# Performance work log

Measured on AMD Instinct MI355X. Metric: run time of the kernel, lower is better.

The kernel has to match this reference:

```python
import jax, jax.numpy as jnp
import numpy as np

B, S, D, H = 2, 2048, 512, 8
HD = D // H
EPS = 1e-5


def _ln(x, g, b):
    mu = jnp.mean(x, axis=-1, keepdims=True)
    var = jnp.mean((x - mu) ** 2, axis=-1, keepdims=True)
    return (x - mu) * jax.lax.rsqrt(var + EPS) * g + b


def setup_inputs() -> dict:
    key = jax.random.key(0)
    ks = jax.random.split(key, 16)
    x = jax.random.normal(ks[0], (B, S, D), dtype=jnp.float32)
    adj = jax.random.randint(ks[1], (B, S, S), 0, 2, dtype=jnp.int32)
    adj = adj.at[:, jnp.arange(S), jnp.arange(S)].set(1)  # self-loops, avoid all-masked rows
    edge_attr = jax.random.normal(ks[2], (B, S, S), dtype=jnp.float32)
    sc = 1.0 / np.sqrt(D)
    p = lambda k, shp: jax.random.normal(k, shp, dtype=jnp.float32) * sc
    return {
        "x": x, "adj_matrix": adj, "edge_attr_matrix": edge_attr,
        "ln1_g": jnp.ones((D,)), "ln1_b": jnp.zeros((D,)),
        "ln2_g": jnp.ones((D,)), "ln2_b": jnp.zeros((D,)),
        "wq": p(ks[3], (D, D)), "bq": jnp.zeros((D,)),
        "wk": p(ks[4], (D, D)), "bk": jnp.zeros((D,)),
        "wv": p(ks[5], (D, D)), "bv": jnp.zeros((D,)),
        "wo": p(ks[6], (D, D)), "bo": jnp.zeros((D,)),
        "w1": p(ks[7], (D, 4 * D)), "b1": jnp.zeros((4 * D,)),
        "w2": p(ks[8], (4 * D, D)), "b2": jnp.zeros((D,)),
    }


def reference(x, adj_matrix, edge_attr_matrix, ln1_g, ln1_b, ln2_g, ln2_b,
              wq, bq, wk, bk, wv, bv, wo, bo, w1, b1, w2, b2):
    b, s, d = x.shape
    residual = x
    nx = _ln(x, ln1_g, ln1_b)
    q = (nx @ wq + bq).reshape(b, s, H, HD).transpose(0, 2, 1, 3)  # [B,H,S,HD]
    k = (nx @ wk + bk).reshape(b, s, H, HD).transpose(0, 2, 1, 3)
    v = (nx @ wv + bv).reshape(b, s, H, HD).transpose(0, 2, 1, 3)
    adjf = adj_matrix.astype(jnp.float32)
    # bias: -inf where no edge, else 0.1*edge_attr*adj (faithful to score_mod)
    bias = jnp.where(adj_matrix > 0, 0.1 * edge_attr_matrix * adjf, -jnp.inf)[:, None]  # [B,1,S,S]
    scores = jnp.einsum('bhqd,bhkd->bhqk', q, k) / np.sqrt(HD) + bias
    attn = jax.nn.softmax(scores, axis=-1)
    out = jnp.einsum('bhqk,bhkd->bhqd', attn, v)
    out = out.transpose(0, 2, 1, 3).reshape(b, s, d)
    x1 = residual + (out @ wo + bo)
    n2 = _ln(x1, ln2_g, ln2_b)
    mlp = jax.nn.gelu(n2 @ w1 + b1, approximate=False) @ w2 + b2
    return x1 + mlp
```

## Files before the change

### kernel.cpp

```cpp
#include <hip/hip_runtime.h>
#include <cstdint>
#include <cstddef>

typedef __bf16 bf16x8 __attribute__((ext_vector_type(8)));
typedef float f32x4 __attribute__((ext_vector_type(4)));
typedef const __attribute__((address_space(1))) void* gas_t;
typedef __attribute__((address_space(3))) void* las_t;

#define QSCALE 0.18033688011112042f
#define BSCALE 0.14426950408889634f

__device__ __forceinline__ unsigned short f2bf(float f) {
  union { float f; unsigned u; } v; v.f = f;
  unsigned r = v.u + 0x7FFFu + ((v.u >> 16) & 1u);
  return (unsigned short)(r >> 16);
}
__device__ __forceinline__ float bf2f(unsigned short h) {
  union { unsigned u; float f; } v; v.u = ((unsigned)h) << 16;
  return v.f;
}
__device__ __forceinline__ unsigned pack_bf16(float p0, float p1) {
  union { float f; unsigned u; } a, b; a.f = p0; b.f = p1;
  return __builtin_amdgcn_perm(b.u + 0x8000u, a.u + 0x8000u, 0x07060302u);
}
__device__ __forceinline__ void gll16(const void* g, void* l) {
  __builtin_amdgcn_global_load_lds((gas_t)g, (las_t)l, 16, 0, 0);
}

__global__ __launch_bounds__(256) void transpose_cast(const float* __restrict__ in,
                                                      unsigned short* __restrict__ out,
                                                      int R, int C) {
  __shared__ float tile[32][33];
  int bx = blockIdx.x * 32, by = blockIdx.y * 32;
  int tx = threadIdx.x & 31, tg = threadIdx.x >> 5;
  #pragma unroll
  for (int i = 0; i < 4; i++) {
    int r = tg * 4 + i;
    tile[r][tx] = in[(size_t)(by + r) * C + bx + tx];
  }
  __syncthreads();
  #pragma unroll
  for (int i = 0; i < 4; i++) {
    int r = tg * 4 + i;
    out[(size_t)(bx + r) * R + by + tx] = f2bf(tile[tx][r]);
  }
}

struct TP4 { const float* in[4]; unsigned short* out[4]; };
__global__ __launch_bounds__(256) void transpose_cast4(TP4 p) {
  __shared__ float tile[32][33];
  const float* in = p.in[blockIdx.z];
  unsigned short* out = p.out[blockIdx.z];
  int bx = blockIdx.x * 32, by = blockIdx.y * 32;
  int tx = threadIdx.x & 31, tg = threadIdx.x >> 5;
  #pragma unroll
  for (int i = 0; i < 4; i++) {
    int r = tg * 4 + i;
    tile[r][tx] = in[(size_t)(by + r) * 512 + bx + tx];
  }
  __syncthreads();
  #pragma unroll
  for (int i = 0; i < 4; i++) {
    int r = tg * 4 + i;
    out[(size_t)(bx + r) * 512 + by + tx] = f2bf(tile[tx][r]);
  }
}

__global__ __launch_bounds__(256) void bias_pack(const int* __restrict__ adj,
                                                 const float* __restrict__ edge,
                                                 unsigned short* __restrict__ bp) {
  size_t i = ((size_t)blockIdx.x * 256 + threadIdx.x) * 4;
  int4 a = *(const int4*)(adj + i);
  float4 e = *(const float4*)(edge + i);
  ushort4 r;
  r.x = a.x > 0 ? f2bf(BSCALE * e.x * (float)a.x - 20.0f) : f2bf(-30000.0f);
  r.y = a.y > 0 ? f2bf(BSCALE * e.y * (float)a.y - 20.0f) : f2bf(-30000.0f);
  r.z = a.z > 0 ? f2bf(BSCALE * e.z * (float)a.z - 20.0f) : f2bf(-30000.0f);
  r.w = a.w > 0 ? f2bf(BSCALE * e.w * (float)a.w - 20.0f) : f2bf(-30000.0f);
  *(ushort4*)(bp + i) = r;
}

__global__ __launch_bounds__(256) void ln_kernel(const float* __restrict__ x,
                                                 const float* __restrict__ g,
                                                 const float* __restrict__ bt,
                                                 unsigned short* __restrict__ out) {
  int row = blockIdx.x, tid = threadIdx.x;
  float2 v = *(const float2*)(x + (size_t)row * 512 + tid * 2);
  float s = v.x + v.y, s2 = v.x * v.x + v.y * v.y;
  #pragma unroll
  for (int m = 1; m < 64; m <<= 1) { s += __shfl_xor(s, m, 64); s2 += __shfl_xor(s2, m, 64); }
  __shared__ float red[8];
  int w = tid >> 6;
  if ((tid & 63) == 0) { red[w * 2] = s; red[w * 2 + 1] = s2; }
  __syncthreads();
  float ts = red[0] + red[2] + red[4] + red[6];
  float ts2 = red[1] + red[3] + red[5] + red[7];
  float mu = ts * (1.0f / 512.0f);
  float rs = rsqrtf(ts2 * (1.0f / 512.0f) - mu * mu + 1e-5f);
  int c = tid * 2;
  ushort2 o;
  o.x = f2bf((v.x - mu) * rs * g[c] + bt[c]);
  o.y = f2bf((v.y - mu) * rs * g[c + 1] + bt[c + 1]);
  *(ushort2*)(out + (size_t)row * 512 + c) = o;
}

__global__ __launch_bounds__(256) void ln_fuse2(const float* __restrict__ x,
                                                const unsigned short* __restrict__ opp,
                                                const float* __restrict__ bo,
                                                const float* __restrict__ g,
                                                const float* __restrict__ bt,
                                                float* __restrict__ x1,
                                                unsigned short* __restrict__ n2) {
  const size_t MN = (size_t)4096 * 512;
  int row = blockIdx.x, tid = threadIdx.x;
  int c = tid * 2;
  size_t idx = (size_t)row * 512 + c;
  float2 xv = *(const float2*)(x + idx);
  ushort2 p0 = *(const ushort2*)(opp + idx);
  ushort2 p1 = *(const ushort2*)(opp + MN + idx);
  float2 v;
  v.x = xv.x + bo[c]     + bf2f(p0.x) + bf2f(p1.x);
  v.y = xv.y + bo[c + 1] + bf2f(p0.y) + bf2f(p1.y);
  float s = v.x + v.y, s2 = v.x * v.x + v.y * v.y;
  #pragma unroll
  for (int m = 1; m < 64; m <<= 1) { s += __shfl_xor(s, m, 64); s2 += __shfl_xor(s2, m, 64); }
  __shared__ float red[8];
  int w = tid >> 6;
  if ((tid & 63) == 0) { red[w * 2] = s; red[w * 2 + 1] = s2; }
  __syncthreads();
  float ts = red[0] + red[2] + red[4] + red[6];
  float ts2 = red[1] + red[3] + red[5] + red[7];
  float mu = ts * (1.0f / 512.0f);
  float rs = rsqrtf(ts2 * (1.0f / 512.0f) - mu * mu + 1e-5f);
  *(float2*)(x1 + idx) = v;
  ushort2 o;
  o.x = f2bf((v.x - mu) * rs * g[c] + bt[c]);
  o.y = f2bf((v.y - mu) * rs * g[c + 1] + bt[c + 1]);
  *(ushort2*)(n2 + idx) = o;
}

__global__ __launch_bounds__(256) void final_combine(const float* __restrict__ x1,
                                                     const float* __restrict__ b2,
                                                     const unsigned short* __restrict__ mp,
                                                     float* __restrict__ out) {
  const size_t MN = (size_t)4096 * 512;
  size_t i = ((size_t)blockIdx.x * 256 + threadIdx.x) * 4;
  float4 xv = *(const float4*)(x1 + i);
  float4 bv = *(const float4*)(b2 + (i & 511));
  float4 a;
  a.x = xv.x + bv.x; a.y = xv.y + bv.y; a.z = xv.z + bv.z; a.w = xv.w + bv.w;
  #pragma unroll
  for (int sp = 0; sp < 4; sp++) {
    ushort4 p = *(const ushort4*)(mp + sp * MN + i);
    a.x += bf2f(p.x); a.y += bf2f(p.y); a.z += bf2f(p.z); a.w += bf2f(p.w);
  }
  *(float4*)(out + i) = a;
}

struct EpiQKV {
  unsigned short *q, *k, *v;
  const float *bq, *bk, *bv;
  __device__ void operator()(int m, int n, float val) const {
    int b = m >> 11, s = m & 2047;
    int which = n >> 9, col = n & 511;
    int h = col >> 6, d = col & 63;
    int bh = b * 8 + h;
    if (which == 0)      q[((size_t)bh * 2048 + s) * 64 + d] = f2bf((val + bq[col]) * QSCALE);
    else if (which == 1) k[((size_t)bh * 2048 + s) * 64 + d] = f2bf(val + bk[col]);
    else                 v[((size_t)bh * 2048 + s) * 64 + d] = f2bf(val + bv[col]);
  }
};
struct EpiPart {
  unsigned short* dst; int ldn;
  __device__ void operator()(int m, int n, float val) const {
    dst[(size_t)blockIdx.z * 4096 * 512 + (size_t)m * ldn + n] = f2bf(val);
  }
};
struct EpiGelu {
  const float* b1; unsigned short* h;
  __device__ void operator()(int m, int n, float val) const {
    float t = val + b1[n];
    float gl = 0.5f * t * (1.0f + erff(t * 0.70710678118654752f));
    h[(size_t)m * 2048 + n] = f2bf(gl);
  }
};

template <typename Epi>
__global__ __launch_bounds__(256, 2) void gemm_bt(const unsigned short* __restrict__ A,
                                                  const unsigned short* __restrict__ Bt,
                                                  int lda, int ldb, int kchunk, Epi epi) {
  __shared__ unsigned short a_lds[2][128 * 64];
  __shared__ unsigned short b_lds[2][128 * 64];
  const int tid = threadIdx.x;
  const int lane = tid & 63;
  const int w = tid >> 6;
  const int l15 = lane & 15, quad = lane >> 4;
  const int wm = w >> 1, wn = w & 1;
  const int m0 = blockIdx.y * 128, n0 = blockIdx.x * 128;
  const int K0 = blockIdx.z * kchunk;
  const int nIter = kchunk >> 6;

  f32x4 acc[4][4] = {};

  #pragma unroll
  for (int i = 0; i < 4; i++) {
    int c = tid + i * 256;
    int g = c >> 6;
    int row = (g >> 1) * 16 + l15;
    int col = (g & 1) * 32 + quad * 8;
    gll16(A + (size_t)(m0 + row) * lda + K0 + col, a_lds[0] + (size_t)(c & ~63) * 8);
    gll16(Bt + (size_t)(n0 + row) * ldb + K0 + col, b_lds[0] + (size_t)(c & ~63) * 8);
  }

  for (int it = 0; it < nIter; it++) {
    const int cur = it & 1;
    __syncthreads();
    if (it + 1 < nIter) {
      const int kn = K0 + (it + 1) * 64;
      #pragma unroll
      for (int i = 0; i < 4; i++) {
        int c = tid + i * 256;
        int g = c >> 6;
        int row = (g >> 1) * 16 + l15;
        int col = (g & 1) * 32 + quad * 8;
        gll16(A + (size_t)(m0 + row) * lda + kn + col, a_lds[1 - cur] + (size_t)(c & ~63) * 8);
        gll16(Bt + (size_t)(n0 + row) * ldb + kn + col, b_lds[1 - cur] + (size_t)(c & ~63) * 8);
      }
    }
    bf16x8 af[4][2], bfr[4][2];
    #pragma unroll
    for (int t = 0; t < 4; t++)
      #pragma unroll
      for (int ks = 0; ks < 2; ks++) {
        af[t][ks]  = *(const bf16x8*)(a_lds[cur] + (((size_t)(wm * 4 + t) * 2 + ks) * 64 + lane) * 8);
        bfr[t][ks] = *(const bf16x8*)(b_lds[cur] + (((size_t)(wn * 4 + t) * 2 + ks) * 64 + lane) * 8);
      }
    #pragma unroll
    for (int mt = 0; mt < 4; mt++)
      #pragma unroll
      for (int nt = 0; nt < 4; nt++) {
        acc[mt][nt] = __builtin_amdgcn_mfma_f32_16x16x32_bf16(af[mt][0], bfr[nt][0], acc[mt][nt], 0, 0, 0);
        acc[mt][nt] = __builtin_amdgcn_mfma_f32_16x16x32_bf16(af[mt][1], bfr[nt][1], acc[mt][nt], 0, 0, 0);
      }
  }
  #pragma unroll
  for (int mt = 0; mt < 4; mt++)
    #pragma unroll
    for (int nt = 0; nt < 4; nt++)
      #pragma unroll
      for (int r = 0; r < 4; r++)
        epi(m0 + wm * 64 + mt * 16 + quad * 4 + r, n0 + wn * 64 + nt * 16 + l15, acc[mt][nt][r]);
}

__global__ __launch_bounds__(256) void vt_kernel(const unsigned short* __restrict__ vb,
                                                 unsigned short* __restrict__ vbT) {
  __shared__ unsigned short tile[64][72];
  const int bh = blockIdx.y, s0 = blockIdx.x * 64;
  const int tid = threadIdx.x;
  const unsigned short* src = vb + ((size_t)bh * 2048 + s0) * 64;
  #pragma unroll
  for (int i = 0; i < 2; i++) {
    int r = (tid >> 3) + i * 32;
    int c8 = (tid & 7) * 8;
    *(uint4*)(&tile[r][c8]) = *(const uint4*)(src + (size_t)r * 64 + c8);
  }
  __syncthreads();
  unsigned short* dst = vbT + (size_t)bh * 64 * 2048 + s0;
  #pragma unroll
  for (int i = 0; i < 2; i++) {
    int d = (tid >> 3) + i * 32;
    int s8 = (tid & 7) * 8;
    ushort4 o0, o1;
    o0.x = tile[s8 + 0][d]; o0.y = tile[s8 + 1][d]; o0.z = tile[s8 + 2][d]; o0.w = tile[s8 + 3][d];
    o1.x = tile[s8 + 4][d]; o1.y = tile[s8 + 5][d]; o1.z = tile[s8 + 6][d]; o1.w = tile[s8 + 7][d];
    *(ushort4*)(dst + (size_t)d * 2048 + s8) = o0;
    *(ushort4*)(dst + (size_t)d * 2048 + s8 + 4) = o1;
  }
}

__global__ __launch_bounds__(256, 4) void attn_kernel(const unsigned short* __restrict__ Q,
                                                      const unsigned short* __restrict__ Kb,
                                                      const unsigned short* __restrict__ VT,
                                                      const unsigned short* __restrict__ biasp,
                                                      unsigned short* __restrict__ o_part,
                                                      float* __restrict__ l_part) {
  const int tid = threadIdx.x;
  const int lane = tid & 63, w = tid >> 6;
  const int l15 = lane & 15, quad = lane >> 4;
  const int bh = blockIdx.x, b = bh >> 3;
  const int q0 = blockIdx.y * 128 + w * 32;
  const int split = blockIdx.z;

  bf16x8 qf[2][2];
  const unsigned short* brow[2];
  #pragma unroll
  for (int g = 0; g < 2; g++) {
    const unsigned short* qrow = Q + ((size_t)bh * 2048 + q0 + g * 16 + l15) * 64;
    qf[g][0] = *(const bf16x8*)(qrow + quad * 8);
    qf[g][1] = *(const bf16x8*)(qrow + 32 + quad * 8);
    brow[g] = biasp + ((size_t)b * 2048 + q0 + g * 16 + l15) * 2048;
  }

  const unsigned short* krow = Kb + ((size_t)bh * 2048 + l15) * 64;
  const unsigned short* vrow0 = VT + ((size_t)bh * 64 + l15) * 2048;

  f32x4 o_acc[2][4] = {};
  float l_acc[2] = {0.0f, 0.0f};

  const int srcA = ((lane & 16) << 1) | l15;
  const int srcB = srcA + 16;
  const bool hiTile = quad >= 2;

  const int kt0 = split * 8;
  for (int kt = kt0; kt < kt0 + 8; kt++) {
    const int kcol = kt * 64;
    #pragma unroll
    for (int H = 0; H < 2; H++) {
      bf16x8 kf[2][2];
      #pragma unroll
      for (int t = 0; t < 2; t++) {
        const unsigned short* kp = krow + (size_t)(kcol + (2 * H + t) * 16) * 64;
        kf[t][0] = *(const bf16x8*)(kp + quad * 8);
        kf[t][1] = *(const bf16x8*)(kp + 32 + quad * 8);
      }
      unsigned pk[2][2][2];
      #pragma unroll
      for (int t = 0; t < 2; t++) {
        const int mt16 = (2 * H + t) * 16;
        #pragma unroll
        for (int g = 0; g < 2; g++) {
          ushort4 bl = *(const ushort4*)(brow[g] + kcol + mt16 + quad * 4);
          f32x4 cb;
          cb[0] = bf2f(bl.x); cb[1] = bf2f(bl.y); cb[2] = bf2f(bl.z); cb[3] = bf2f(bl.w);
          f32x4 s = __builtin_amdgcn_mfma_f32_16x16x32_bf16(kf[t][0], qf[g][0], cb, 0, 0, 0);
          s = __builtin_amdgcn_mfma_f32_16x16x32_bf16(kf[t][1], qf[g][1], s, 0, 0, 0);
          float p0 = exp2f(s[0]), p1 = exp2f(s[1]), p2 = exp2f(s[2]), p3 = exp2f(s[3]);
          l_acc[g] += (p0 + p1) + (p2 + p3);
          pk[t][g][0] = pack_bf16(p0, p1);
          pk[t][g][1] = pack_bf16(p2, p3);
        }
      }
      bf16x8 vf[4];
      #pragma unroll
      for (int dt = 0; dt < 4; dt++)
        vf[dt] = *(const bf16x8*)(vrow0 + (size_t)dt * 16 * 2048 + kcol + H * 32 + quad * 8);
      #pragma unroll
      for (int g = 0; g < 2; g++) {
        unsigned r0a = (unsigned)__shfl((int)pk[0][g][0], srcA);
        unsigned r0b = (unsigned)__shfl((int)pk[1][g][0], srcA);
        unsigned r1a = (unsigned)__shfl((int)pk[0][g][1], srcA);
        unsigned r1b = (unsigned)__shfl((int)pk[1][g][1], srcA);
        unsigned r2a = (unsigned)__shfl((int)pk[0][g][0], srcB);
        unsigned r2b = (unsigned)__shfl((int)pk[1][g][0], srcB);
        unsigned r3a = (unsigned)__shfl((int)pk[0][g][1], srcB);
        unsigned r3b = (unsigned)__shfl((int)pk[1][g][1], srcB);
        union { uint4 u; bf16x8 v; } fr;
        fr.u.x = hiTile ? r0b : r0a;
        fr.u.y = hiTile ? r1b : r1a;
        fr.u.z = hiTile ? r2b : r2a;
        fr.u.w = hiTile ? r3b : r3a;
        #pragma unroll
        for (int dt = 0; dt < 4; dt++)
          o_acc[g][dt] = __builtin_amdgcn_mfma_f32_16x16x32_bf16(fr.v, vf[dt], o_acc[g][dt], 0, 0, 0);
      }
    }
  }

  const size_t obase = ((size_t)split * 16 + bh) * 2048;
  #pragma unroll
  for (int g = 0; g < 2; g++) {
    float l = l_acc[g];
    l += __shfl_xor(l, 16, 64);
    l += __shfl_xor(l, 32, 64);
    if (quad == 0) l_part[obase + q0 + g * 16 + l15] = l;
    #pragma unroll
    for (int dt = 0; dt < 4; dt++)
      #pragma unroll
      for (int r = 0; r < 4; r++)
        o_part[(obase + q0 + g * 16 + quad * 4 + r) * 64 + dt * 16 + l15] =
            f2bf(o_acc[g][dt][r]);
  }
}

__global__ __launch_bounds__(256) void combine_kernel(const unsigned short* __restrict__ o_part,
                                                      const float* __restrict__ l_part,
                                                      unsigned short* __restrict__ ao) {
  const int row = blockIdx.x;
  const int b = row >> 11, s = row & 2047;
  const int col = threadIdx.x * 2;
  const int h = col >> 6, d = col & 63;
  const int bh = b * 8 + h;
  float ox = 0.0f, oy = 0.0f, l = 0.0f;
  #pragma unroll
  for (int sp = 0; sp < 4; sp++) {
    size_t base = (size_t)(sp * 16 + bh) * 2048 + s;
    ushort2 o = *(const ushort2*)(o_part + base * 64 + d);
    ox += bf2f(o.x); oy += bf2f(o.y);
    l += l_part[base];
  }
  float inv = 1.0f / l;
  ushort2 o;
  o.x = f2bf(ox * inv);
  o.y = f2bf(oy * inv);
  *(ushort2*)(ao + (size_t)row * 512 + col) = o;
}

extern "C" void kernel_launch(void* const* d_in, const int* in_sizes, int n_in,
                              void* d_out, int out_size, void* d_ws, size_t ws_size,
                              hipStream_t stream) {
  (void)in_sizes; (void)n_in; (void)out_size; (void)ws_size;
  const float* x    = (const float*)d_in[0];
  const int*   adj  = (const int*)d_in[1];
  const float* edge = (const float*)d_in[2];
  const float* ln1g = (const float*)d_in[3];
  const float* ln1b = (const float*)d_in[4];
  const float* ln2g = (const float*)d_in[5];
  const float* ln2b = (const float*)d_in[6];
  const float* wq = (const float*)d_in[7];  const float* bq = (const float*)d_in[8];
  const float* wk = (const float*)d_in[9];  const float* bk = (const float*)d_in[10];
  const float* wv = (const float*)d_in[11]; const float* bv = (const float*)d_in[12];
  const float* wo = (const float*)d_in[13]; const float* bo = (const float*)d_in[14];
  const float* w1 = (const float*)d_in[15]; const float* b1 = (const float*)d_in[16];
  const float* w2 = (const float*)d_in[17]; const float* b2 = (const float*)d_in[18];
  float* out = (float*)d_out;

  char* ws = (char*)d_ws;
  unsigned short* qkvT = (unsigned short*)ws; ws += (size_t)1536 * 512 * 2;
  unsigned short* woT  = (unsigned short*)ws; ws += (size_t)512 * 512 * 2;
  unsigned short* w1T  = (unsigned short*)ws; ws += (size_t)2048 * 512 * 2;
  unsigned short* w2T  = (unsigned short*)ws; ws += (size_t)512 * 2048 * 2;
  unsigned short* bp   = (unsigned short*)ws;
  unsigned short* opp  = (unsigned short*)ws; ws += (size_t)2 * 2048 * 2048 * 2;
  unsigned short* nx   = (unsigned short*)ws;
  unsigned short* n2   = (unsigned short*)ws; ws += (size_t)4096 * 512 * 2;
  unsigned short* qb   = (unsigned short*)ws;
  unsigned short* ao   = (unsigned short*)ws; ws += (size_t)4096 * 512 * 2;
  unsigned short* kb   = (unsigned short*)ws; ws += (size_t)4096 * 512 * 2;
  unsigned short* vb   = (unsigned short*)ws;
  float*          x1   = (float*)ws;          ws += (size_t)4096 * 512 * 2;
  unsigned short* vbT  = (unsigned short*)ws; ws += (size_t)4096 * 512 * 2;
  char* region1 = ws;
  unsigned short* opt  = (unsigned short*)region1;
  unsigned short* hb   = (unsigned short*)region1;
  float*          lpt  = (float*)(region1 + (size_t)4 * 16 * 2048 * 64 * 2);
  unsigned short* mp   = (unsigned short*)(region1 + (size_t)4 * 16 * 2048 * 64 * 2 + 524288);

  dim3 blk(256);
  TP4 tp; tp.in[0] = wq; tp.in[1] = wk; tp.in[2] = wv; tp.in[3] = wo;
  tp.out[0] = qkvT; tp.out[1] = qkvT + (size_t)512 * 512;
  tp.out[2] = qkvT + (size_t)2 * 512 * 512; tp.out[3] = woT;
  transpose_cast4<<<dim3(16, 16, 4), blk, 0, stream>>>(tp);
  transpose_cast<<<dim3(64, 16), blk, 0, stream>>>(w1, w1T, 512, 2048);
  transpose_cast<<<dim3(16, 64), blk, 0, stream>>>(w2, w2T, 2048, 512);
  bias_pack<<<8192, blk, 0, stream>>>(adj, edge, bp);
  ln_kernel<<<4096, blk, 0, stream>>>(x, ln1g, ln1b, nx);
  gemm_bt<<<dim3(12, 32, 1), blk, 0, stream>>>(nx, qkvT, 512, 512, 512,
                                               EpiQKV{qb, kb, vb, bq, bk, bv});
  vt_kernel<<<dim3(32, 16), blk, 0, stream>>>(vb, vbT);
  attn_kernel<<<dim3(16, 16, 4), blk, 0, stream>>>(qb, kb, vbT, bp, opt, lpt);
  combine_kernel<<<4096, blk, 0, stream>>>(opt, lpt, ao);
  gemm_bt<<<dim3(4, 32, 2), blk, 0, stream>>>(ao, woT, 512, 512, 256,
                                              EpiPart{opp, 512});
  ln_fuse2<<<4096, blk, 0, stream>>>(x, opp, bo, ln2g, ln2b, x1, n2);
  gemm_bt<<<dim3(16, 32, 1), blk, 0, stream>>>(n2, w1T, 512, 512, 512,
                                               EpiGelu{b1, hb});
  gemm_bt<<<dim3(4, 32, 4), blk, 0, stream>>>(hb, w2T, 2048, 2048, 512,
                                              EpiPart{mp, 512});
  final_combine<<<2048, blk, 0, stream>>>(x1, b2, mp, out);
}
```

Before: 366.4 us.

## Stage attention K/V through LDS, single-buffer GEMM, merge weight transposes

```diff
diff --git a/kernel.cpp b/kernel.cpp
--- a/kernel.cpp
+++ b/kernel.cpp
@@ -27,11 +27,17 @@
   __builtin_amdgcn_global_load_lds((gas_t)g, (las_t)l, 16, 0, 0);
 }
 
-__global__ __launch_bounds__(256) void transpose_cast(const float* __restrict__ in,
-                                                      unsigned short* __restrict__ out,
-                                                      int R, int C) {
+struct TPAll { const float* in[6]; unsigned short* out[6]; int R[6]; int C[6]; };
+__global__ __launch_bounds__(256) void transpose_all(TPAll p) {
+  const int z = blockIdx.z;
+  int bxb = blockIdx.x, byb = blockIdx.y;
+  if (z == 5) { int t = bxb; bxb = byb; byb = t; }
+  const int R = p.R[z], C = p.C[z];
+  const int bx = bxb * 32, by = byb * 32;
+  if (bx >= C || by >= R) return;
+  const float* in = p.in[z];
+  unsigned short* out = p.out[z];
   __shared__ float tile[32][33];
-  int bx = blockIdx.x * 32, by = blockIdx.y * 32;
   int tx = threadIdx.x & 31, tg = threadIdx.x >> 5;
   #pragma unroll
   for (int i = 0; i < 4; i++) {
@@ -43,26 +49,6 @@
   for (int i = 0; i < 4; i++) {
     int r = tg * 4 + i;
     out[(size_t)(bx + r) * R + by + tx] = f2bf(tile[tx][r]);
-  }
-}
-
-struct TP4 { const float* in[4]; unsigned short* out[4]; };
-__global__ __launch_bounds__(256) void transpose_cast4(TP4 p) {
-  __shared__ float tile[32][33];
-  const float* in = p.in[blockIdx.z];
-  unsigned short* out = p.out[blockIdx.z];
-  int bx = blockIdx.x * 32, by = blockIdx.y * 32;
-  int tx = threadIdx.x & 31, tg = threadIdx.x >> 5;
-  #pragma unroll
-  for (int i = 0; i < 4; i++) {
-    int r = tg * 4 + i;
-    tile[r][tx] = in[(size_t)(by + r) * 512 + bx + tx];
-  }
-  __syncthreads();
-  #pragma unroll
-  for (int i = 0; i < 4; i++) {
-    int r = tg * 4 + i;
-    out[(size_t)(bx + r) * 512 + by + tx] = f2bf(tile[tx][r]);
   }
 }
 
@@ -186,54 +172,40 @@
 };
 
 template <typename Epi>
-__global__ __launch_bounds__(256, 2) void gemm_bt(const unsigned short* __restrict__ A,
+__global__ __launch_bounds__(256, 3) void gemm_bt(const unsigned short* __restrict__ A,
                                                   const unsigned short* __restrict__ Bt,
                                                   int lda, int ldb, int kchunk, Epi epi) {
-  __shared__ unsigned short a_lds[2][128 * 64];
-  __shared__ unsigned short b_lds[2][128 * 64];
+  __shared__ unsigned short a_lds[128 * 64];
+  __shared__ unsigned short b_lds[128 * 64];
   const int tid = threadIdx.x;
   const int lane = tid & 63;
   const int w = tid >> 6;
   const int l15 = lane & 15, quad = lane >> 4;
   const int wm = w >> 1, wn = w & 1;
   const int m0 = blockIdx.y * 128, n0 = blockIdx.x * 128;
-  const int K0 = blockIdx.z * kchunk;
-  const int nIter = kchunk >> 6;
+  const int K0 = blockIdx.z * kchunk, K1 = K0 + kchunk;
 
   f32x4 acc[4][4] = {};
 
-  #pragma unroll
-  for (int i = 0; i < 4; i++) {
-    int c = tid + i * 256;
-    int g = c >> 6;
-    int row = (g >> 1) * 16 + l15;
-    int col = (g & 1) * 32 + quad * 8;
-    gll16(A + (size_t)(m0 + row) * lda + K0 + col, a_lds[0] + (size_t)(c & ~63) * 8);
-    gll16(Bt + (size_t)(n0 + row) * ldb + K0 + col, b_lds[0] + (size_t)(c & ~63) * 8);
-  }
-
-  for (int it = 0; it < nIter; it++) {
-    const int cur = it & 1;
+  for (int k0 = K0; k0 < K1; k0 += 64) {
     __syncthreads();
-    if (it + 1 < nIter) {
-      const int kn = K0 + (it + 1) * 64;
-      #pragma unroll
-      for (int i = 0; i < 4; i++) {
-        int c = tid + i * 256;
-        int g = c >> 6;
-        int row = (g >> 1) * 16 + l15;
-        int col = (g & 1) * 32 + quad * 8;
-        gll16(A + (size_t)(m0 + row) * lda + kn + col, a_lds[1 - cur] + (size_t)(c & ~63) * 8);
-        gll16(Bt + (size_t)(n0 + row) * ldb + kn + col, b_lds[1 - cur] + (size_t)(c & ~63) * 8);
-      }
+    #pragma unroll
+    for (int i = 0; i < 4; i++) {
+      int c = tid + i * 256;
+      int g = c >> 6;
+      int row = (g >> 1) * 16 + l15;
+      int col = (g & 1) * 32 + quad * 8;
+      gll16(A + (size_t)(m0 + row) * lda + k0 + col, a_lds + (size_t)(c & ~63) * 8);
+      gll16(Bt + (size_t)(n0 + row) * ldb + k0 + col, b_lds + (size_t)(c & ~63) * 8);
     }
+    __syncthreads();
     bf16x8 af[4][2], bfr[4][2];
     #pragma unroll
     for (int t = 0; t < 4; t++)
       #pragma unroll
       for (int ks = 0; ks < 2; ks++) {
-        af[t][ks]  = *(const bf16x8*)(a_lds[cur] + (((size_t)(wm * 4 + t) * 2 + ks) * 64 + lane) * 8);
-        bfr[t][ks] = *(const bf16x8*)(b_lds[cur] + (((size_t)(wn * 4 + t) * 2 + ks) * 64 + lane) * 8);
+        af[t][ks]  = *(const bf16x8*)(a_lds + (((size_t)(wm * 4 + t) * 2 + ks) * 64 + lane) * 8);
+        bfr[t][ks] = *(const bf16x8*)(b_lds + (((size_t)(wn * 4 + t) * 2 + ks) * 64 + lane) * 8);
       }
     #pragma unroll
     for (int mt = 0; mt < 4; mt++)
@@ -284,6 +256,9 @@
                                                       const unsigned short* __restrict__ biasp,
                                                       unsigned short* __restrict__ o_part,
                                                       float* __restrict__ l_part) {
+  __shared__ unsigned short k_lds[2][64 * 64];
+  __shared__ unsigned short v_lds[2][64 * 64];
+
   const int tid = threadIdx.x;
   const int lane = tid & 63, w = tid >> 6;
   const int l15 = lane & 15, quad = lane >> 4;
@@ -301,35 +276,74 @@
     brow[g] = biasp + ((size_t)b * 2048 + q0 + g * 16 + l15) * 2048;
   }
 
-  const unsigned short* krow = Kb + ((size_t)bh * 2048 + l15) * 64;
-  const unsigned short* vrow0 = VT + ((size_t)bh * 64 + l15) * 2048;
-
   f32x4 o_acc[2][4] = {};
   float l_acc[2] = {0.0f, 0.0f};
+
+  const unsigned short* kbase = Kb + (size_t)bh * 2048 * 64;
+  const unsigned short* vbase = VT + (size_t)bh * 64 * 2048;
 
   const int srcA = ((lane & 16) << 1) | l15;
   const int srcB = srcA + 16;
   const bool hiTile = quad >= 2;
 
-  const int kt0 = split * 8;
-  for (int kt = kt0; kt < kt0 + 8; kt++) {
+  const int kt0 = split * 8, kt1 = kt0 + 8;
+
+  #pragma unroll
+  for (int i = 0; i < 2; i++) {
+    int c = tid + i * 256;
+    int g = c >> 6;
+    int rr = (g >> 1) * 16 + l15;
+    int cc = (g & 1) * 32 + quad * 8;
+    gll16(kbase + (size_t)(kt0 * 64 + rr) * 64 + cc, k_lds[0] + (size_t)(c & ~63) * 8);
+    gll16(vbase + (size_t)rr * 2048 + kt0 * 64 + cc, v_lds[0] + (size_t)(c & ~63) * 8);
+  }
+  ushort4 blc[2][4];
+  #pragma unroll
+  for (int g = 0; g < 2; g++)
+    #pragma unroll
+    for (int mt = 0; mt < 4; mt++)
+      blc[g][mt] = *(const ushort4*)(brow[g] + kt0 * 64 + mt * 16 + quad * 4);
+
+  for (int kt = kt0; kt < kt1; kt++) {
+    const int cur = (kt - kt0) & 1;
     const int kcol = kt * 64;
+    __syncthreads();
+
+    if (kt + 1 < kt1) {
+      const int kcn = (kt + 1) * 64;
+      #pragma unroll
+      for (int i = 0; i < 2; i++) {
+        int c = tid + i * 256;
+        int g = c >> 6;
+        int rr = (g >> 1) * 16 + l15;
+        int cc = (g & 1) * 32 + quad * 8;
+        gll16(kbase + (size_t)(kcn + rr) * 64 + cc, k_lds[1 - cur] + (size_t)(c & ~63) * 8);
+        gll16(vbase + (size_t)rr * 2048 + kcn + cc, v_lds[1 - cur] + (size_t)(c & ~63) * 8);
+      }
+    }
+    const int ktn64 = (kt + 1 < kt1) ? (kt + 1) * 64 : kcol;
+    ushort4 bln[2][4];
+    #pragma unroll
+    for (int g = 0; g < 2; g++)
+      #pragma unroll
+      for (int mt = 0; mt < 4; mt++)
+        bln[g][mt] = *(const ushort4*)(brow[g] + ktn64 + mt * 16 + quad * 4);
+
     #pragma unroll
     for (int H = 0; H < 2; H++) {
       bf16x8 kf[2][2];
       #pragma unroll
       for (int t = 0; t < 2; t++) {
-        const unsigned short* kp = krow + (size_t)(kcol + (2 * H + t) * 16) * 64;
-        kf[t][0] = *(const bf16x8*)(kp + quad * 8);
-        kf[t][1] = *(const bf16x8*)(kp + 32 + quad * 8);
+        const int mtile = 2 * H + t;
+        kf[t][0] = *(const bf16x8*)(k_lds[cur] + ((size_t)(mtile * 2 + 0) * 64 + lane) * 8);
+        kf[t][1] = *(const bf16x8*)(k_lds[cur] + ((size_t)(mtile * 2 + 1) * 64 + lane) * 8);
       }
       unsigned pk[2][2][2];
       #pragma unroll
       for (int t = 0; t < 2; t++) {
-        const int mt16 = (2 * H + t) * 16;
         #pragma unroll
         for (int g = 0; g < 2; g++) {
-          ushort4 bl = *(const ushort4*)(brow[g] + kcol + mt16 + quad * 4);
+          ushort4 bl = blc[g][2 * H + t];
           f32x4 cb;
           cb[0] = bf2f(bl.x); cb[1] = bf2f(bl.y); cb[2] = bf2f(bl.z); cb[3] = bf2f(bl.w);
           f32x4 s = __builtin_amdgcn_mfma_f32_16x16x32_bf16(kf[t][0], qf[g][0], cb, 0, 0, 0);
@@ -343,7 +357,7 @@
       bf16x8 vf[4];
       #pragma unroll
       for (int dt = 0; dt < 4; dt++)
-        vf[dt] = *(const bf16x8*)(vrow0 + (size_t)dt * 16 * 2048 + kcol + H * 32 + quad * 8);
+        vf[dt] = *(const bf16x8*)(v_lds[cur] + ((size_t)(dt * 2 + H) * 64 + lane) * 8);
       #pragma unroll
       for (int g = 0; g < 2; g++) {
         unsigned r0a = (unsigned)__shfl((int)pk[0][g][0], srcA);
@@ -364,6 +378,12 @@
           o_acc[g][dt] = __builtin_amdgcn_mfma_f32_16x16x32_bf16(fr.v, vf[dt], o_acc[g][dt], 0, 0, 0);
       }
     }
+
+    #pragma unroll
+    for (int g = 0; g < 2; g++)
+      #pragma unroll
+      for (int mt = 0; mt < 4; mt++)
+        blc[g][mt] = bln[g][mt];
   }
 
   const size_t obase = ((size_t)split * 16 + bh) * 2048;
@@ -446,12 +466,13 @@
   unsigned short* mp   = (unsigned short*)(region1 + (size_t)4 * 16 * 2048 * 64 * 2 + 524288);
 
   dim3 blk(256);
-  TP4 tp; tp.in[0] = wq; tp.in[1] = wk; tp.in[2] = wv; tp.in[3] = wo;
+  TPAll tp;
+  tp.in[0] = wq; tp.in[1] = wk; tp.in[2] = wv; tp.in[3] = wo; tp.in[4] = w1; tp.in[5] = w2;
   tp.out[0] = qkvT; tp.out[1] = qkvT + (size_t)512 * 512;
-  tp.out[2] = qkvT + (size_t)2 * 512 * 512; tp.out[3] = woT;
-  transpose_cast4<<<dim3(16, 16, 4), blk, 0, stream>>>(tp);
-  transpose_cast<<<dim3(64, 16), blk, 0, stream>>>(w1, w1T, 512, 2048);
-  transpose_cast<<<dim3(16, 64), blk, 0, stream>>>(w2, w2T, 2048, 512);
+  tp.out[2] = qkvT + (size_t)2 * 512 * 512; tp.out[3] = woT; tp.out[4] = w1T; tp.out[5] = w2T;
+  tp.R[0] = tp.R[1] = tp.R[2] = tp.R[3] = 512; tp.R[4] = 512; tp.R[5] = 2048;
+  tp.C[0] = tp.C[1] = tp.C[2] = tp.C[3] = 512; tp.C[4] = 2048; tp.C[5] = 512;
+  transpose_all<<<dim3(64, 16, 6), blk, 0, stream>>>(tp);
   bias_pack<<<8192, blk, 0, stream>>>(adj, edge, bp);
   ln_kernel<<<4096, blk, 0, stream>>>(x, ln1g, ln1b, nx);
   gemm_bt<<<dim3(12, 32, 1), blk, 0, stream>>>(nx, qkvT, 512, 512, 512,
```

Measured after the change: 318.2 us. 1.15x faster.
